# Kernel tuning notes

Measured on AMD Instinct MI355X. Metric: run time of the kernel, lower is better.

## Reference

```python
import jax, jax.numpy as jnp
import numpy as np

N = 50000      # nodes
E = 800000     # edges (avg degree 16)
IN = 128       # in_channels
OUT = 128      # out_channels
H1, C1 = 4, 64 # conv1: 4 heads x 64 -> concat 256
H2, C2 = 1, OUT
NEG_SLOPE = 0.2


def setup_inputs() -> dict:
    key = jax.random.key(0)
    ks = jax.random.split(key, 10)
    def glorot(k, shape, fan):
        return jax.random.normal(k, shape, jnp.float32) * (1.0 / np.sqrt(fan))
    x = jax.random.normal(ks[0], (N, IN), jnp.float32)
    edge_index = jax.random.randint(ks[1], (2, E), 0, N)
    W1 = glorot(ks[2], (IN, H1 * C1), IN)
    att_src1 = glorot(ks[3], (H1, C1), C1)
    att_dst1 = glorot(ks[4], (H1, C1), C1)
    b1 = jnp.zeros((H1 * C1,), jnp.float32)
    W2 = glorot(ks[5], (H1 * C1, H2 * C2), H1 * C1)
    att_src2 = glorot(ks[6], (H2, C2), C2)
    att_dst2 = glorot(ks[7], (H2, C2), C2)
    b2 = jnp.zeros((OUT,), jnp.float32)
    return {"x": x, "edge_index": edge_index,
            "W1": W1, "att_src1": att_src1, "att_dst1": att_dst1, "b1": b1,
            "W2": W2, "att_src2": att_src2, "att_dst2": att_dst2, "b2": b2}


def gat_conv(x, src, dst, W, att_s, att_d, bias, heads, ch):
    """PyG GATConv: linear -> edge attention -> per-dst softmax -> scatter-sum."""
    n = x.shape[0]
    h = (x @ W).reshape(n, heads, ch)                      # [N, H, C]
    a_s = jnp.einsum('nhc,hc->nh', h, att_s)               # [N, H]
    a_d = jnp.einsum('nhc,hc->nh', h, att_d)               # [N, H]
    e = jax.nn.leaky_relu(a_s[src] + a_d[dst], NEG_SLOPE)  # [Etot, H]
    e_max = jax.ops.segment_max(e, dst, num_segments=n)    # [N, H]
    e = jnp.exp(e - e_max[dst])
    denom = jax.ops.segment_sum(e, dst, num_segments=n)    # [N, H]
    alpha = e / (denom[dst] + 1e-16)                        # [Etot, H]
    msg = h[src] * alpha[:, :, None]                        # [Etot, H, C]
    out = jax.ops.segment_sum(msg, dst, num_segments=n)     # [N, H, C]
    return out.reshape(n, heads * ch) + bias


def reference(x, edge_index, W1, att_src1, att_dst1, b1, W2, att_src2, att_dst2, b2):
    n = x.shape[0]
    loop = jnp.arange(n)
    # GATConv(add_self_loops=True): append (i, i) edges
    src = jnp.concatenate([edge_index[0], loop])
    dst = jnp.concatenate([edge_index[1], loop])
    h = jax.nn.relu(gat_conv(x, src, dst, W1, att_src1, att_dst1, b1, H1, C1))
    out = jax.nn.relu(gat_conv(h, src, dst, W2, att_src2, att_dst2, b2, H2, C2))
    return out
```

## Files before the change

### kernel.cpp

```cpp
#include <hip/hip_runtime.h>
#include <hip/hip_bf16.h>
#include <hip/hip_fp16.h>


#define NEG_SLOPE 0.2f

typedef __attribute__((ext_vector_type(8))) _Float16 f16x8;
typedef __attribute__((ext_vector_type(8))) short s16x8;
typedef __attribute__((ext_vector_type(4))) float f32x4;

__device__ inline void loadH8(float* v, const __half* p) {
    union { s16x8 raw; __half2 h2[4]; } u;
    u.raw = *(const s16x8*)p;
#pragma unroll
    for (int i = 0; i < 4; ++i) {
        float2 f = __half22float2(u.h2[i]);
        v[2 * i] = f.x;
        v[2 * i + 1] = f.y;
    }
}


__device__ inline void pack_w_elem(const float* __restrict__ W, __half* __restrict__ bp,
                                   int K, int N, int tid) {
    int k = tid / N, n = tid - k * N;
    int ks = k >> 5, k5 = k & 31, quad = k5 >> 3, j = k5 & 7;
    int ct = n >> 4;
    int lane = quad * 16 + (n & 15);
    size_t idx = ((size_t)(ct * (K >> 5) + ks) * 64 + lane) * 8 + j;
    bp[idx] = __float2half(W[tid]);
}

__global__ __launch_bounds__(256) void prep_kernel(
        const float* __restrict__ x, __half* __restrict__ xf, int nx,
        const float* __restrict__ W1, __half* __restrict__ bp1,
        const float* __restrict__ W2, __half* __restrict__ bp2,
        const int* __restrict__ ei, int E, int* __restrict__ cnt,
        int* __restrict__ rank, int N) {
    int tid = blockIdx.x * blockDim.x + threadIdx.x;
    if (tid < nx) xf[tid] = __float2half(x[tid]);
    int Etot = E + N;
    if (tid < Etot) {
        int d = (tid < E) ? ei[E + tid] : (tid - E);
        rank[tid] = atomicAdd(&cnt[d], 1);
    }
    if (tid < 128 * 256) pack_w_elem(W1, bp1, 128, 256, tid);
    if (tid < 256 * 128) pack_w_elem(W2, bp2, 256, 128, tid);
}


__global__ __launch_bounds__(256) void scan_chained(
        const int* __restrict__ cnt, int* __restrict__ row_start,
        unsigned long long* __restrict__ status,
        int* __restrict__ bcount, int N, int nb) {
    __shared__ int sm[256];
    __shared__ int sbid;
    __shared__ int sprefix;
    int t = threadIdx.x;
    if (t == 0) sbid = atomicAdd(bcount, 1);
    __syncthreads();
    const int bid = sbid;
    int i = bid * 256 + t;
    int c = (i < N) ? cnt[i] : 0;
    sm[t] = c;
    __syncthreads();
    for (int off = 1; off < 256; off <<= 1) {
        int v = (t >= off) ? sm[t - off] : 0;
        __syncthreads();
        sm[t] += v;
        __syncthreads();
    }
    int incl = sm[t];
    int aggregate = sm[255];
    if (t == 0) {
        unsigned long long pub = (bid == 0)
            ? (((unsigned long long)aggregate << 2) | 2ull)
            : (((unsigned long long)aggregate << 2) | 1ull);
        __hip_atomic_store(&status[bid], pub, __ATOMIC_RELEASE, __HIP_MEMORY_SCOPE_AGENT);
        int prefix = 0;
        if (bid > 0) {
            int j = bid - 1;
            while (true) {
                unsigned long long s =
                    __hip_atomic_load(&status[j], __ATOMIC_ACQUIRE, __HIP_MEMORY_SCOPE_AGENT);
                unsigned long long f = s & 3ull;
                if (f == 0ull) continue;
                prefix += (int)(s >> 2);
                if (f == 2ull) break;
                --j;
            }
            __hip_atomic_store(&status[bid],
                (((unsigned long long)(prefix + aggregate)) << 2) | 2ull,
                __ATOMIC_RELEASE, __HIP_MEMORY_SCOPE_AGENT);
        }
        sprefix = prefix;
    }
    __syncthreads();
    int base = sprefix;
    if (i < N) row_start[i] = base + incl - c;
    if (bid == nb - 1 && t == 255) row_start[N] = base + aggregate;
}


template<int K, int NN, int H, bool ATOMIC>
__device__ void gemm_body(int bx, int M,
        const __half* __restrict__ A, const __half* __restrict__ Bp,
        const float* __restrict__ att_s, const float* __restrict__ att_d,
        float* __restrict__ as_, float* __restrict__ ad_,
        __half* __restrict__ Hout) {
    constexpr int KS = K >> 5;
    constexpr int CW = NN / 64;
    constexpr int RW = 4 / CW;
    constexpr int C = NN / H;
    const int lane = threadIdx.x & 63;
    const int w = threadIdx.x >> 6;
    const int wr = w / CW;
    const int wc = w % CW;
    const int quad = lane >> 4;
    const int r16 = lane & 15;
    const int mBase = bx * (RW * 32) + wr * 32;
    const int nBase = wc * 64;
    const int head = nBase / C;

    f32x4 acc[2][4];
#pragma unroll
    for (int rt = 0; rt < 2; ++rt)
#pragma unroll
        for (int ct = 0; ct < 4; ++ct) acc[rt][ct] = (f32x4){0.f, 0.f, 0.f, 0.f};

#pragma unroll
    for (int ks = 0; ks < KS; ++ks) {
        f16x8 af[2];
#pragma unroll
        for (int rt = 0; rt < 2; ++rt) {
            int row = mBase + rt * 16 + r16;
            if (row < M) {
                size_t off = (size_t)row * K + ks * 32 + quad * 8;
                af[rt] = *(const f16x8*)(A + off);
            } else {
                af[rt] = (f16x8){0,0,0,0,0,0,0,0};
            }
        }
        f16x8 bf[4];
#pragma unroll
        for (int ct = 0; ct < 4; ++ct) {
            int ctg = (nBase >> 4) + ct;
            size_t off = ((size_t)(ctg * KS + ks) * 64 + lane) * 8;
            bf[ct] = *(const f16x8*)(Bp + off);
        }
#pragma unroll
        for (int rt = 0; rt < 2; ++rt)
#pragma unroll
            for (int ct = 0; ct < 4; ++ct)
                acc[rt][ct] = __builtin_amdgcn_mfma_f32_16x16x32_f16(af[rt], bf[ct], acc[rt][ct], 0, 0, 0);
    }

#pragma unroll
    for (int rt = 0; rt < 2; ++rt)
#pragma unroll
        for (int ct = 0; ct < 4; ++ct) {
            int row0 = mBase + rt * 16 + quad * 4;
            int col = nBase + ct * 16 + r16;
#pragma unroll
            for (int r = 0; r < 4; ++r) {
                int row = row0 + r;
                if (row < M) Hout[(size_t)row * NN + col] = __float2half(acc[rt][ct][r]);
            }
        }

    float attS[4], attD[4];
#pragma unroll
    for (int ct = 0; ct < 4; ++ct) {
        int cc = (nBase % C) + ct * 16 + r16;
        attS[ct] = att_s[head * C + cc];
        attD[ct] = att_d[head * C + cc];
    }
#pragma unroll
    for (int rt = 0; rt < 2; ++rt)
#pragma unroll
        for (int r = 0; r < 4; ++r) {
            float ps = 0.f, pd = 0.f;
#pragma unroll
            for (int ct = 0; ct < 4; ++ct) {
                ps += acc[rt][ct][r] * attS[ct];
                pd += acc[rt][ct][r] * attD[ct];
            }
#pragma unroll
            for (int off = 1; off < 16; off <<= 1) {
                ps += __shfl_xor(ps, off);
                pd += __shfl_xor(pd, off);
            }
            int row = mBase + rt * 16 + quad * 4 + r;
            if (r16 == 0 && row < M) {
                if (ATOMIC) {
                    atomicAdd(&as_[row * H + head], ps);
                    atomicAdd(&ad_[row * H + head], pd);
                } else {
                    as_[row * H + head] = ps;
                    ad_[row * H + head] = pd;
                }
            }
        }
}

template<int K, int NN, int H, bool ATOMIC>
__global__ __launch_bounds__(256) void mfma_gemm(int M,
        const __half* __restrict__ A, const __half* __restrict__ Bp,
        const float* __restrict__ att_s, const float* __restrict__ att_d,
        float* __restrict__ as_, float* __restrict__ ad_,
        __half* __restrict__ Hout) {
    gemm_body<K, NN, H, ATOMIC>(blockIdx.x, M, A, Bp, att_s, att_d, as_, ad_, Hout);
}


__global__ __launch_bounds__(256) void fill_gemm1(
        int FB, const int* __restrict__ ei, int E, int N,
        const int* __restrict__ row_start, const int* __restrict__ rank,
        int* __restrict__ csr_src,
        const __half* __restrict__ A, const __half* __restrict__ Bp,
        const float* __restrict__ att_s, const float* __restrict__ att_d,
        float* __restrict__ as_, float* __restrict__ ad_,
        __half* __restrict__ Hout) {
    if ((int)blockIdx.x < FB) {
        int e = blockIdx.x * 256 + threadIdx.x;
        int Etot = E + N;
        if (e >= Etot) return;
        int s, d;
        if (e < E) { s = ei[e]; d = ei[E + e]; } else { s = e - E; d = s; }
        csr_src[row_start[d] + rank[e]] = s;
        return;
    }
    gemm_body<128, 256, 4, false>(blockIdx.x - FB, N, A, Bp,
                                  att_s, att_d, as_, ad_, Hout);
}


__device__ inline float edge_w(float a) {
    float e = a > 0.f ? a : NEG_SLOPE * a;
    return __expf(e);
}

template<int U, int HC, int H, int GRP>
__device__ inline void agg_step(int p, const int* __restrict__ csr_src,
                                const __half* __restrict__ h,
                                const float* __restrict__ as_, float adv,
                                int c0, int head, float* acc, float& den) {
    int srcv[U];
#pragma unroll
    for (int u = 0; u < U; ++u) srcv[u] = csr_src[p + u * GRP];
    float f[U][8];
#pragma unroll
    for (int u = 0; u < U; ++u) loadH8(f[u], h + (size_t)srcv[u] * HC + c0);
    float wv[U];
#pragma unroll
    for (int u = 0; u < U; ++u) wv[u] = edge_w(as_[srcv[u] * H + head] + adv);
#pragma unroll
    for (int u = 0; u < U; ++u) den += wv[u];
#pragma unroll
    for (int u = 0; u < U; ++u)
#pragma unroll
        for (int i = 0; i < 8; ++i) acc[i] += wv[u] * f[u][i];
}

template<int HC, int H, bool F16OUT>
__global__ __launch_bounds__(256) void fused_agg(int N,
                                                 const int* __restrict__ row_start,
                                                 const int* __restrict__ csr_src,
                                                 const __half* __restrict__ h,
                                                 const float* __restrict__ as_,
                                                 const float* __restrict__ ad_,
                                                 const float* __restrict__ bias,
                                                 float* __restrict__ out,
                                                 __half* __restrict__ outh) {
    constexpr int LPE = HC / 8;
    constexpr int GRP = 64 / LPE;
    constexpr int C = HC / H;
    const int n = blockIdx.x * 4 + (threadIdx.x >> 6);
    if (n >= N) return;
    const int lane = threadIdx.x & 63;
    const int g = lane / LPE;
    const int lq = lane % LPE;
    const int c0 = lq * 8;
    const int head = c0 / C;
    const int s0 = row_start[n], s1 = row_start[n + 1];
    const float adv = ad_[n * H + head];
    float acc[8] = {};
    float den = 0.f;
    int p = s0 + g;
    for (; p + 3 * GRP < s1; p += 4 * GRP)
        agg_step<4, HC, H, GRP>(p, csr_src, h, as_, adv, c0, head, acc, den);
    for (; p < s1; p += GRP)
        agg_step<1, HC, H, GRP>(p, csr_src, h, as_, adv, c0, head, acc, den);
#pragma unroll
    for (int off = LPE; off < 64; off <<= 1) {
        den += __shfl_xor(den, off);
#pragma unroll
        for (int i = 0; i < 8; ++i) acc[i] += __shfl_xor(acc[i], off);
    }
    if (g == 0) {
        float dinv = 1.0f / (den + 1e-16f);
        float o[8];
#pragma unroll
        for (int i = 0; i < 8; ++i) {
            float v = acc[i] * dinv + bias[c0 + i];
            o[i] = v > 0.f ? v : 0.f;
        }
        if (F16OUT) {
            union { s16x8 raw; __half hv[8]; } u;
#pragma unroll
            for (int i = 0; i < 8; ++i) u.hv[i] = __float2half(o[i]);
            *(s16x8*)(outh + (size_t)n * HC + c0) = u.raw;
        } else {
            float4 v0 = make_float4(o[0], o[1], o[2], o[3]);
            float4 v1 = make_float4(o[4], o[5], o[6], o[7]);
            *(float4*)(out + (size_t)n * HC + c0) = v0;
            *(float4*)(out + (size_t)n * HC + c0 + 4) = v1;
        }
    }
}

extern "C" void kernel_launch(void* const* d_in, const int* in_sizes, int n_in,
                              void* d_out, int out_size, void* d_ws, size_t ws_size,
                              hipStream_t stream) {
    const float* x      = (const float*)d_in[0];
    const int*   ei     = (const int*)d_in[1];
    const float* W1     = (const float*)d_in[2];
    const float* att_s1 = (const float*)d_in[3];
    const float* att_d1 = (const float*)d_in[4];
    const float* b1     = (const float*)d_in[5];
    const float* W2     = (const float*)d_in[6];
    const float* att_s2 = (const float*)d_in[7];
    const float* att_d2 = (const float*)d_in[8];
    const float* b2     = (const float*)d_in[9];
    float* out = (float*)d_out;

    const int N_ = in_sizes[0] / 128;
    const int E_ = in_sizes[1] / 2;
    const int Etot = E_ + N_;

    __half* h1 = (__half*)d_ws;
    __half* x2 = h1 + (size_t)N_ * 256;
    __half* xf = x2;
    __half* bp1 = x2 + (size_t)N_ * 256;
    __half* bp2 = bp1 + 32768;
    float* as1 = (float*)(bp2 + 32768);
    float* ad1 = as1 + (size_t)N_ * 4;
    int*   cnt    = (int*)(ad1 + (size_t)N_ * 4);
    float* as2    = (float*)(cnt + N_);
    float* ad2    = as2 + N_;
    int*   bcount = (int*)(ad2 + N_);
    unsigned long long* status = (unsigned long long*)(bcount + 2);
    size_t zeroBytes = (size_t)(3 * N_ + 2) * 4 + 256 * 8;
    int* row_start = (int*)(status + 256);
    int* rank      = row_start + (N_ + 1);
    int* csr_src   = rank + Etot;

    int nb = (N_ + 255) / 256;
    int FB = (Etot + 255) / 256;
    int G1B = (N_ + 31) / 32;
    int nx = N_ * 128;

    hipMemsetAsync(cnt, 0, zeroBytes, stream);
    prep_kernel<<<(nx + 255) / 256, 256, 0, stream>>>(
        x, xf, nx, W1, bp1, W2, bp2, ei, E_, cnt, rank, N_);
    scan_chained<<<nb, 256, 0, stream>>>(cnt, row_start, status, bcount, N_, nb);

    fill_gemm1<<<FB + G1B, 256, 0, stream>>>(
        FB, ei, E_, N_, row_start, rank, csr_src,
        xf, bp1, att_s1, att_d1, as1, ad1, h1);
    fused_agg<256, 4, true><<<(N_ + 3) / 4, 256, 0, stream>>>(
        N_, row_start, csr_src, h1, as1, ad1, b1, nullptr, x2);

    __half* h2 = h1;
    mfma_gemm<256, 128, 1, true><<<(N_ + 63) / 64, 256, 0, stream>>>(
        N_, x2, bp2, att_s2, att_d2, as2, ad2, h2);
    fused_agg<128, 1, false><<<(N_ + 3) / 4, 256, 0, stream>>>(
        N_, row_start, csr_src, h2, as2, ad2, b2, out, nullptr);

    (void)n_in; (void)out_size; (void)ws_size;
}
```

Before: 318.2 us.

## Aggregate raw features before the per-head projection in layer one

Layer one now computes the attention scores from the GEMM but no longer stores the projected features. Instead it aggregates the 128-wide fp16 input rows per destination with per-head softmax weights into a [N,4,128] buffer, then runs a per-head MFMA GEMM with a repacked W1, adding bias and ReLU. This relies on linearity to halve the bytes gathered per edge (128 instead of 256 halves). In exchange it writes and re-reads a larger intermediate and adds an extra kernel launch.

```diff
diff --git a/kernel.cpp b/kernel.cpp
--- a/kernel.cpp
+++ b/kernel.cpp
@@ -31,9 +31,21 @@
     bp[idx] = __float2half(W[tid]);
 }
 
+__device__ inline void pack_w1b_elem(const float* __restrict__ W1, __half* __restrict__ bp,
+                                     int tid) {
+    int k = tid >> 8, n = tid & 255;
+    int h = n >> 6, c = n & 63;
+    int ct = c >> 4, ks = k >> 5, k5 = k & 31, quad = k5 >> 3, j = k5 & 7;
+    int lane = quad * 16 + (c & 15);
+    size_t idx = ((size_t)((h * 4 + ct) * 4 + ks) * 64 + lane) * 8 + j;
+    bp[idx] = __float2half(W1[tid]);
+}
+
+
 __global__ __launch_bounds__(256) void prep_kernel(
         const float* __restrict__ x, __half* __restrict__ xf, int nx,
         const float* __restrict__ W1, __half* __restrict__ bp1,
+        __half* __restrict__ bp1b,
         const float* __restrict__ W2, __half* __restrict__ bp2,
         const int* __restrict__ ei, int E, int* __restrict__ cnt,
         int* __restrict__ rank, int N) {
@@ -44,8 +56,11 @@
         int d = (tid < E) ? ei[E + tid] : (tid - E);
         rank[tid] = atomicAdd(&cnt[d], 1);
     }
-    if (tid < 128 * 256) pack_w_elem(W1, bp1, 128, 256, tid);
-    if (tid < 256 * 128) pack_w_elem(W2, bp2, 256, 128, tid);
+    if (tid < 128 * 256) {
+        pack_w_elem(W1, bp1, 128, 256, tid);
+        pack_w1b_elem(W1, bp1b, tid);
+        pack_w_elem(W2, bp2, 256, 128, tid);
+    }
 }
 
 
@@ -102,7 +117,7 @@
 }
 
 
-template<int K, int NN, int H, bool ATOMIC>
+template<int K, int NN, int H, bool ATOMIC, bool WRITEH>
 __device__ void gemm_body(int bx, int M,
         const __half* __restrict__ A, const __half* __restrict__ Bp,
         const float* __restrict__ att_s, const float* __restrict__ att_d,
@@ -155,18 +170,20 @@
                 acc[rt][ct] = __builtin_amdgcn_mfma_f32_16x16x32_f16(af[rt], bf[ct], acc[rt][ct], 0, 0, 0);
     }
 
-#pragma unroll
-    for (int rt = 0; rt < 2; ++rt)
-#pragma unroll
-        for (int ct = 0; ct < 4; ++ct) {
-            int row0 = mBase + rt * 16 + quad * 4;
-            int col = nBase + ct * 16 + r16;
-#pragma unroll
-            for (int r = 0; r < 4; ++r) {
-                int row = row0 + r;
-                if (row < M) Hout[(size_t)row * NN + col] = __float2half(acc[rt][ct][r]);
-            }
-        }
+    if (WRITEH) {
+#pragma unroll
+        for (int rt = 0; rt < 2; ++rt)
+#pragma unroll
+            for (int ct = 0; ct < 4; ++ct) {
+                int row0 = mBase + rt * 16 + quad * 4;
+                int col = nBase + ct * 16 + r16;
+#pragma unroll
+                for (int r = 0; r < 4; ++r) {
+                    int row = row0 + r;
+                    if (row < M) Hout[(size_t)row * NN + col] = __float2half(acc[rt][ct][r]);
+                }
+            }
+    }
 
     float attS[4], attD[4];
 #pragma unroll
@@ -203,13 +220,13 @@
         }
 }
 
-template<int K, int NN, int H, bool ATOMIC>
+template<int K, int NN, int H, bool ATOMIC, bool WRITEH>
 __global__ __launch_bounds__(256) void mfma_gemm(int M,
         const __half* __restrict__ A, const __half* __restrict__ Bp,
         const float* __restrict__ att_s, const float* __restrict__ att_d,
         float* __restrict__ as_, float* __restrict__ ad_,
         __half* __restrict__ Hout) {
-    gemm_body<K, NN, H, ATOMIC>(blockIdx.x, M, A, Bp, att_s, att_d, as_, ad_, Hout);
+    gemm_body<K, NN, H, ATOMIC, WRITEH>(blockIdx.x, M, A, Bp, att_s, att_d, as_, ad_, Hout);
 }
 
 
@@ -219,8 +236,7 @@
         int* __restrict__ csr_src,
         const __half* __restrict__ A, const __half* __restrict__ Bp,
         const float* __restrict__ att_s, const float* __restrict__ att_d,
-        float* __restrict__ as_, float* __restrict__ ad_,
-        __half* __restrict__ Hout) {
+        float* __restrict__ as_, float* __restrict__ ad_) {
     if ((int)blockIdx.x < FB) {
         int e = blockIdx.x * 256 + threadIdx.x;
         int Etot = E + N;
@@ -230,8 +246,8 @@
         csr_src[row_start[d] + rank[e]] = s;
         return;
     }
-    gemm_body<128, 256, 4, false>(blockIdx.x - FB, N, A, Bp,
-                                  att_s, att_d, as_, ad_, Hout);
+    gemm_body<128, 256, 4, false, false>(blockIdx.x - FB, N, A, Bp,
+                                         att_s, att_d, as_, ad_, nullptr);
 }
 
 
@@ -239,6 +255,137 @@
     float e = a > 0.f ? a : NEG_SLOPE * a;
     return __expf(e);
 }
+
+template<int U>
+__device__ inline void aggx_step(int p, const int* __restrict__ csr_src,
+                                 const __half* __restrict__ xf,
+                                 const float* __restrict__ as_,
+                                 const float* adv, int c0,
+                                 float acc[4][8], float* den) {
+    int srcv[U];
+#pragma unroll
+    for (int u = 0; u < U; ++u) srcv[u] = csr_src[p + u * 4];
+    float xv[U][8];
+#pragma unroll
+    for (int u = 0; u < U; ++u) loadH8(xv[u], xf + (size_t)srcv[u] * 128 + c0);
+    float asv[U][4];
+#pragma unroll
+    for (int u = 0; u < U; ++u) *(float4*)asv[u] = *(const float4*)(as_ + srcv[u] * 4);
+#pragma unroll
+    for (int u = 0; u < U; ++u)
+#pragma unroll
+        for (int h = 0; h < 4; ++h) {
+            float wgt = edge_w(asv[u][h] + adv[h]);
+            den[h] += wgt;
+#pragma unroll
+            for (int i = 0; i < 8; ++i) acc[h][i] += wgt * xv[u][i];
+        }
+}
+
+__global__ __launch_bounds__(256) void agg1x(int N,
+        const int* __restrict__ row_start, const int* __restrict__ csr_src,
+        const __half* __restrict__ xf,
+        const float* __restrict__ as_, const float* __restrict__ ad_,
+        __half* __restrict__ xagg) {
+    const int n = blockIdx.x * 4 + (threadIdx.x >> 6);
+    if (n >= N) return;
+    const int lane = threadIdx.x & 63;
+    const int g = lane >> 4;
+    const int lq = lane & 15;
+    const int c0 = lq * 8;
+    const int s0 = row_start[n], s1 = row_start[n + 1];
+    float adv[4];
+    *(float4*)adv = *(const float4*)(ad_ + n * 4);
+    float acc[4][8] = {};
+    float den[4] = {};
+    int p = s0 + g;
+    for (; p + 12 < s1; p += 16)
+        aggx_step<4>(p, csr_src, xf, as_, adv, c0, acc, den);
+    for (; p < s1; p += 4)
+        aggx_step<1>(p, csr_src, xf, as_, adv, c0, acc, den);
+#pragma unroll
+    for (int off = 16; off < 64; off <<= 1) {
+#pragma unroll
+        for (int h = 0; h < 4; ++h) {
+            den[h] += __shfl_xor(den[h], off);
+#pragma unroll
+            for (int i = 0; i < 8; ++i) acc[h][i] += __shfl_xor(acc[h][i], off);
+        }
+    }
+    if (g == 0) {
+#pragma unroll
+        for (int h = 0; h < 4; ++h) {
+            float dinv = 1.0f / (den[h] + 1e-16f);
+            union { s16x8 raw; __half hv[8]; } u;
+#pragma unroll
+            for (int i = 0; i < 8; ++i) u.hv[i] = __float2half(acc[h][i] * dinv);
+            *(s16x8*)(xagg + (size_t)n * 512 + h * 128 + c0) = u.raw;
+        }
+    }
+}
+
+
+__global__ __launch_bounds__(256) void gemm1b(int M,
+        const __half* __restrict__ xagg, const __half* __restrict__ bp1b,
+        const float* __restrict__ b1, __half* __restrict__ x2) {
+    const int lane = threadIdx.x & 63;
+    const int head = threadIdx.x >> 6;
+    const int quad = lane >> 4;
+    const int r16 = lane & 15;
+    const int mBase = blockIdx.x * 32;
+
+    f32x4 acc[2][4];
+#pragma unroll
+    for (int rt = 0; rt < 2; ++rt)
+#pragma unroll
+        for (int ct = 0; ct < 4; ++ct) acc[rt][ct] = (f32x4){0.f, 0.f, 0.f, 0.f};
+
+#pragma unroll
+    for (int ks = 0; ks < 4; ++ks) {
+        f16x8 af[2];
+#pragma unroll
+        for (int rt = 0; rt < 2; ++rt) {
+            int row = mBase + rt * 16 + r16;
+            if (row < M) {
+                size_t off = (size_t)row * 512 + head * 128 + ks * 32 + quad * 8;
+                af[rt] = *(const f16x8*)(xagg + off);
+            } else {
+                af[rt] = (f16x8){0,0,0,0,0,0,0,0};
+            }
+        }
+        f16x8 bf[4];
+#pragma unroll
+        for (int ct = 0; ct < 4; ++ct) {
+            size_t off = ((size_t)((head * 4 + ct) * 4 + ks) * 64 + lane) * 8;
+            bf[ct] = *(const f16x8*)(bp1b + off);
+        }
+#pragma unroll
+        for (int rt = 0; rt < 2; ++rt)
+#pragma unroll
+            for (int ct = 0; ct < 4; ++ct)
+                acc[rt][ct] = __builtin_amdgcn_mfma_f32_16x16x32_f16(af[rt], bf[ct], acc[rt][ct], 0, 0, 0);
+    }
+
+    float bias[4];
+#pragma unroll
+    for (int ct = 0; ct < 4; ++ct) bias[ct] = b1[head * 64 + ct * 16 + r16];
+#pragma unroll
+    for (int rt = 0; rt < 2; ++rt)
+#pragma unroll
+        for (int ct = 0; ct < 4; ++ct) {
+            int row0 = mBase + rt * 16 + quad * 4;
+            int col = head * 64 + ct * 16 + r16;
+#pragma unroll
+            for (int r = 0; r < 4; ++r) {
+                int row = row0 + r;
+                if (row < M) {
+                    float o = acc[rt][ct][r] + bias[ct];
+                    x2[(size_t)row * 256 + col] = __float2half(o > 0.f ? o : 0.f);
+                }
+            }
+        }
+}
+
 
 template<int U, int HC, int H, int GRP>
 __device__ inline void agg_step(int p, const int* __restrict__ csr_src,
@@ -262,7 +409,7 @@
         for (int i = 0; i < 8; ++i) acc[i] += wv[u] * f[u][i];
 }
 
-template<int HC, int H, bool F16OUT>
+template<int HC, int H>
 __global__ __launch_bounds__(256) void fused_agg(int N,
                                                  const int* __restrict__ row_start,
                                                  const int* __restrict__ csr_src,
@@ -270,8 +417,7 @@
                                                  const float* __restrict__ as_,
                                                  const float* __restrict__ ad_,
                                                  const float* __restrict__ bias,
-                                                 float* __restrict__ out,
-                                                 __half* __restrict__ outh) {
+                                                 float* __restrict__ out) {
     constexpr int LPE = HC / 8;
     constexpr int GRP = 64 / LPE;
     constexpr int C = HC / H;
@@ -305,17 +451,10 @@
             float v = acc[i] * dinv + bias[c0 + i];
             o[i] = v > 0.f ? v : 0.f;
         }
-        if (F16OUT) {
-            union { s16x8 raw; __half hv[8]; } u;
-#pragma unroll
-            for (int i = 0; i < 8; ++i) u.hv[i] = __float2half(o[i]);
-            *(s16x8*)(outh + (size_t)n * HC + c0) = u.raw;
-        } else {
-            float4 v0 = make_float4(o[0], o[1], o[2], o[3]);
-            float4 v1 = make_float4(o[4], o[5], o[6], o[7]);
-            *(float4*)(out + (size_t)n * HC + c0) = v0;
-            *(float4*)(out + (size_t)n * HC + c0 + 4) = v1;
-        }
+        float4 v0 = make_float4(o[0], o[1], o[2], o[3]);
+        float4 v1 = make_float4(o[4], o[5], o[6], o[7]);
+        *(float4*)(out + (size_t)n * HC + c0) = v0;
+        *(float4*)(out + (size_t)n * HC + c0 + 4) = v1;
     }
 }
 
@@ -338,11 +477,13 @@
     const int E_ = in_sizes[1] / 2;
     const int Etot = E_ + N_;
 
-    __half* h1 = (__half*)d_ws;
-    __half* x2 = h1 + (size_t)N_ * 256;
-    __half* xf = x2;
-    __half* bp1 = x2 + (size_t)N_ * 256;
-    __half* bp2 = bp1 + 32768;
+    __half* xagg = (__half*)d_ws;
+    __half* h2   = xagg;
+    __half* x2   = xagg + (size_t)N_ * 512;
+    __half* xf   = x2;
+    __half* bp1  = x2 + (size_t)N_ * 256;
+    __half* bp1b = bp1 + 32768;
+    __half* bp2  = bp1b + 32768;
     float* as1 = (float*)(bp2 + 32768);
     float* ad1 = as1 + (size_t)N_ * 4;
     int*   cnt    = (int*)(ad1 + (size_t)N_ * 4);
@@ -362,20 +503,20 @@
 
     hipMemsetAsync(cnt, 0, zeroBytes, stream);
     prep_kernel<<<(nx + 255) / 256, 256, 0, stream>>>(
-        x, xf, nx, W1, bp1, W2, bp2, ei, E_, cnt, rank, N_);
+        x, xf, nx, W1, bp1, bp1b, W2, bp2, ei, E_, cnt, rank, N_);
     scan_chained<<<nb, 256, 0, stream>>>(cnt, row_start, status, bcount, N_, nb);
 
     fill_gemm1<<<FB + G1B, 256, 0, stream>>>(
         FB, ei, E_, N_, row_start, rank, csr_src,
-        xf, bp1, att_s1, att_d1, as1, ad1, h1);
-    fused_agg<256, 4, true><<<(N_ + 3) / 4, 256, 0, stream>>>(
-        N_, row_start, csr_src, h1, as1, ad1, b1, nullptr, x2);
-
-    __half* h2 = h1;
-    mfma_gemm<256, 128, 1, true><<<(N_ + 63) / 64, 256, 0, stream>>>(
+        xf, bp1, att_s1, att_d1, as1, ad1);
+    agg1x<<<(N_ + 3) / 4, 256, 0, stream>>>(
+        N_, row_start, csr_src, xf, as1, ad1, xagg);
+    gemm1b<<<(N_ + 31) / 32, 256, 0, stream>>>(N_, xagg, bp1b, b1, x2);
+
+    mfma_gemm<256, 128, 1, true, true><<<(N_ + 63) / 64, 256, 0, stream>>>(
         N_, x2, bp2, att_s2, att_d2, as2, ad2, h2);
-    fused_agg<128, 1, false><<<(N_ + 3) / 4, 256, 0, stream>>>(
-        N_, row_start, csr_src, h2, as2, ad2, b2, out, nullptr);
+    fused_agg<128, 1><<<(N_ + 3) / 4, 256, 0, stream>>>(
+        N_, row_start, csr_src, h2, as2, ad2, b2, out);
 
     (void)n_in; (void)out_size; (void)ws_size;
 }
```

New measurement: 336.2 us. 5.7% more time.
